# Optimization experiments

Hardware: AMD Instinct MI355X
Metric: run time of the kernel (lower is better)

## Reference

```python
import jax, jax.numpy as jnp
import numpy as np

N = 4096
Q_DIM = K_DIM = V_DIM = OUT_DIM = ATTN_DIM = 512
NUM_HEADS = 8
HEAD_DIM = ATTN_DIM // NUM_HEADS
SCALE = float(HEAD_DIM) ** (-0.5)


def setup_inputs() -> dict:
    key = jax.random.key(0)
    ks = jax.random.split(key, 12)
    def lin(kw, kb, out_d, in_d):
        bound = 1.0 / np.sqrt(in_d)
        w = jax.random.uniform(kw, (out_d, in_d), jnp.float32, -bound, bound)
        b = jax.random.uniform(kb, (out_d,), jnp.float32, -bound, bound)
        return w, b
    wq_w, wq_b = lin(ks[0], ks[1], ATTN_DIM, Q_DIM)
    wk_w, wk_b = lin(ks[2], ks[3], ATTN_DIM, K_DIM)
    wv_w, wv_b = lin(ks[4], ks[5], ATTN_DIM, V_DIM)
    wo_w, wo_b = lin(ks[6], ks[7], OUT_DIM, ATTN_DIM)
    q = jax.random.normal(ks[8], (N, Q_DIM), jnp.float32)
    k = jax.random.normal(ks[9], (N, K_DIM), jnp.float32)
    v = jax.random.normal(ks[10], (N, V_DIM), jnp.float32)
    mask = jax.random.uniform(ks[11], (N, N)) < 0.1  # True = masked out
    return {"q": q, "k": k, "v": v, "mask": mask,
            "wq_w": wq_w, "wq_b": wq_b, "wk_w": wk_w, "wk_b": wk_b,
            "wv_w": wv_w, "wv_b": wv_b, "wo_w": wo_w, "wo_b": wo_b}


def reference(q, k, v, mask, wq_w, wq_b, wk_w, wk_b, wv_w, wv_b, wo_w, wo_b):
    # Linear projections (torch Linear: x @ W.T + b)
    qp = q @ wq_w.T + wq_b  # (N, A)
    kp = k @ wk_w.T + wk_b
    vp = v @ wv_w.T + wv_b
    # (N, A) -> (H, N, dh)
    qh = qp.reshape(N, NUM_HEADS, HEAD_DIM).transpose(1, 0, 2)
    kh = kp.reshape(N, NUM_HEADS, HEAD_DIM).transpose(1, 0, 2)
    vh = vp.reshape(N, NUM_HEADS, HEAD_DIM).transpose(1, 0, 2)
    attn = jnp.einsum('hnd,hmd->hnm', qh, kh) * SCALE  # (H, N, N)
    attn = jnp.where(mask[None, :, :], jnp.float32(-1e6), attn)
    attn = jax.nn.softmax(attn, axis=-1)
    o = jnp.einsum('hnm,hmd->hnd', attn, vh)  # (H, N, dh)
    o = o.transpose(1, 0, 2).reshape(N, ATTN_DIM)
    return o @ wo_w.T + wo_b  # (N, out_dim)
```

## Files before the change

kernel.cpp:

```cpp
#include <hip/hip_runtime.h>


typedef __attribute__((ext_vector_type(8))) short bf16x8;
typedef __attribute__((ext_vector_type(4))) float f32x4;

#define N_TOK 4096
#define D_MODEL 512
#define QSCALE 0.18033688f

__device__ __forceinline__ unsigned short f2bf(float f) {
  unsigned u = __float_as_uint(f);
  return (unsigned short)((u + 0x7FFFu + ((u >> 16) & 1u)) >> 16);
}
__device__ __forceinline__ unsigned pack_bf16(float a, float b) {
  unsigned ua = __float_as_uint(a), ub = __float_as_uint(b);
  ua += 0x7FFFu + ((ua >> 16) & 1u);
  ub += 0x7FFFu + ((ub >> 16) & 1u);
  return (ua >> 16) | (ub & 0xFFFF0000u);
}
__device__ __forceinline__ f32x4 mfma16(bf16x8 a, bf16x8 b, f32x4 c) {
  return __builtin_amdgcn_mfma_f32_16x16x32_bf16(a, b, c, 0, 0, 0);
}
__device__ __forceinline__ float fast_exp2(float x) {
#if __has_builtin(__builtin_amdgcn_exp2f)
  return __builtin_amdgcn_exp2f(x);
#else
  return exp2f(x);
#endif
}

__global__ __launch_bounds__(256) void detect_kernel(
    const unsigned* __restrict__ mask, unsigned* __restrict__ flags) {
  __shared__ int s_bad;
  int t = threadIdx.x;
  if (t == 0) s_bad = 0;
  __syncthreads();
  int bad = 0;
  for (int i = t; i < 4096; i += 256)
    if (mask[i] > 1u) bad = 1;
  if (bad) atomicOr(&s_bad, 1);
  __syncthreads();
  if (t == 0) {
    flags[0] = 0;
    flags[1] = s_bad ? 1u : 0u;
  }
}

__global__ __launch_bounds__(256) void pack_mask_kernel(
    const void* __restrict__ m, unsigned long long* __restrict__ bits,
    const unsigned* __restrict__ flags) {
  int gt = blockIdx.x * 256 + threadIdx.x;
  int wave = gt >> 6;
  int lane = threadIdx.x & 63;
  int base = wave * 256;
  unsigned long long b0, b1, b2, b3;
  if (flags[1]) {
    const unsigned char* m8 = (const unsigned char*)m;
    b0 = __ballot(m8[base + 0 * 64 + lane] != 0);
    b1 = __ballot(m8[base + 1 * 64 + lane] != 0);
    b2 = __ballot(m8[base + 2 * 64 + lane] != 0);
    b3 = __ballot(m8[base + 3 * 64 + lane] != 0);
  } else {
    const int* m4 = (const int*)m;
    b0 = __ballot(m4[base + 0 * 64 + lane] != 0);
    b1 = __ballot(m4[base + 1 * 64 + lane] != 0);
    b2 = __ballot(m4[base + 2 * 64 + lane] != 0);
    b3 = __ballot(m4[base + 3 * 64 + lane] != 0);
  }
  if (lane < 4) {
    unsigned long long bl = lane == 0 ? b0 : lane == 1 ? b1 : lane == 2 ? b2 : b3;
    bits[wave * 4 + lane] = bl;
  }
}

template <int F32>
__device__ __forceinline__ void load16(const void* base, int idx,
                                       unsigned short* dst) {
  if (F32) {
    const float* p = (const float*)base + idx;
    float4 f0 = *(const float4*)(p + 0);
    float4 f1 = *(const float4*)(p + 4);
    float4 f2 = *(const float4*)(p + 8);
    float4 f3 = *(const float4*)(p + 12);
    unsigned* d = (unsigned*)dst;
    d[0] = pack_bf16(f0.x, f0.y); d[1] = pack_bf16(f0.z, f0.w);
    d[2] = pack_bf16(f1.x, f1.y); d[3] = pack_bf16(f1.z, f1.w);
    d[4] = pack_bf16(f2.x, f2.y); d[5] = pack_bf16(f2.z, f2.w);
    d[6] = pack_bf16(f3.x, f3.y); d[7] = pack_bf16(f3.z, f3.w);
  } else {
    const unsigned short* p = (const unsigned short*)base + idx;
    *(uint4*)dst = *(const uint4*)p;
    *(uint4*)(dst + 8) = *(const uint4*)(p + 8);
  }
}

template <int A32, int O32>
__device__ __forceinline__ void gemm_body(
    const void* __restrict__ A, const float* __restrict__ W,
    const float* __restrict__ bias, void* __restrict__ out, float oscale) {
  __shared__ unsigned short As[128 * 72];
  __shared__ unsigned short Bs[128 * 72];
  const int t = threadIdx.x;
  const int lane = t & 63, w = t >> 6;
  const int wm = w & 1, wn = w >> 1;
  const int q4 = lane >> 4, i15 = lane & 15;
  const int m0 = blockIdx.y * 128, n0 = blockIdx.x * 128;
  f32x4 acc[4][4] = {};
  const int sr = t >> 2;
  const int sc = (t & 3) * 16;
  for (int k0 = 0; k0 < 512; k0 += 64) {
    __syncthreads();
#pragma unroll
    for (int p = 0; p < 2; ++p) {
      int row = sr + p * 64;
      unsigned short ta[16], tb[16];
      load16<A32>(A, (m0 + row) * 512 + k0 + sc, ta);
      load16<1>(W, (n0 + row) * 512 + k0 + sc, tb);
      *(uint4*)(As + row * 72 + sc) = *(uint4*)ta;
      *(uint4*)(As + row * 72 + sc + 8) = *(uint4*)(ta + 8);
      *(uint4*)(Bs + row * 72 + sc) = *(uint4*)tb;
      *(uint4*)(Bs + row * 72 + sc + 8) = *(uint4*)(tb + 8);
    }
    __syncthreads();
#pragma unroll
    for (int ks = 0; ks < 2; ++ks) {
      bf16x8 af[4], bfr[4];
#pragma unroll
      for (int mt = 0; mt < 4; ++mt)
        af[mt] = *(const bf16x8*)(As + (wm * 64 + mt * 16 + i15) * 72 + q4 * 8 + ks * 32);
#pragma unroll
      for (int nt = 0; nt < 4; ++nt)
        bfr[nt] = *(const bf16x8*)(Bs + (wn * 64 + nt * 16 + i15) * 72 + q4 * 8 + ks * 32);
#pragma unroll
      for (int mt = 0; mt < 4; ++mt)
#pragma unroll
        for (int nt = 0; nt < 4; ++nt)
          acc[mt][nt] = mfma16(af[mt], bfr[nt], acc[mt][nt]);
    }
  }
#pragma unroll
  for (int nt = 0; nt < 4; ++nt) {
    int col = n0 + wn * 64 + nt * 16 + i15;
    float bv = bias[col];
#pragma unroll
    for (int mt = 0; mt < 4; ++mt) {
      int rowb = m0 + wm * 64 + mt * 16 + q4 * 4;
#pragma unroll
      for (int rr = 0; rr < 4; ++rr) {
        int idx = (rowb + rr) * 512 + col;
        float val = (acc[mt][nt][rr] + bv) * oscale;
        if (O32) ((float*)out)[idx] = val;
        else ((unsigned short*)out)[idx] = f2bf(val);
      }
    }
  }
}

__global__ __launch_bounds__(256) void qkv_gemm_kernel(
    const float* __restrict__ q, const float* __restrict__ k,
    const float* __restrict__ v, const float* __restrict__ wq,
    const float* __restrict__ wk, const float* __restrict__ wv,
    const float* __restrict__ bq, const float* __restrict__ bk,
    const float* __restrict__ bv, unsigned short* __restrict__ outbase) {
  int z = blockIdx.z;
  const float* A = z == 0 ? q : z == 1 ? k : v;
  const float* W = z == 0 ? wq : z == 1 ? wk : wv;
  const float* B = z == 0 ? bq : z == 1 ? bk : bv;
  float sc = z == 0 ? QSCALE : 1.0f;
  gemm_body<1, 0>(A, W, B, outbase + (size_t)z * (N_TOK * D_MODEL), sc);
}

__global__ __launch_bounds__(256) void out_gemm_kernel(
    const unsigned short* __restrict__ A, const float* __restrict__ W,
    const float* __restrict__ B, float* __restrict__ out) {
  gemm_body<0, 1>(A, W, B, out, 1.0f);
}

__global__ __launch_bounds__(256, 3) void attn_kernel(
    const unsigned short* __restrict__ qp, const unsigned short* __restrict__ kp,
    const unsigned short* __restrict__ vp,
    const unsigned long long* __restrict__ mbits,
    float* __restrict__ Op, float* __restrict__ dp) {
  __shared__ unsigned short Ks[128 * 64];
  __shared__ unsigned short Vt[64 * 128];
  const int t = threadIdx.x;
  const int lane = t & 63, w = t >> 6;
  const int q4 = lane >> 4, i15 = lane & 15;
  const int head = blockIdx.y;
  const int ch = head * 64;
  const int i0 = blockIdx.x * 128;
  const int iw = w * 32;
  const int bz = blockIdx.z;
  const int t0 = bz * 11;
  const int ntile = (bz < 2) ? 11 : 10;
  const int L0 = i15 + ((q4 & 1) << 5);
  const int L1 = L0 + 16;
  const bool oddsel = q4 >= 2;
  bf16x8 qf[2][2];
#pragma unroll
  for (int nt = 0; nt < 2; ++nt) {
    int ig = i0 + iw + nt * 16 + i15;
#pragma unroll
    for (int ksd = 0; ksd < 2; ++ksd)
      qf[nt][ksd] = *(const bf16x8*)(qp + ig * 512 + ch + q4 * 8 + ksd * 32);
  }
  const unsigned long long* mrow[2];
  mrow[0] = mbits + (size_t)(i0 + iw + i15) * 64;
  mrow[1] = mbits + (size_t)(i0 + iw + 16 + i15) * 64;
  f32x4 oacc[4][2] = {};
  float den[2] = {0.f, 0.f};
  for (int jt = 0; jt < ntile; ++jt) {
    const int j0 = (t0 + jt) * 128;
    __syncthreads();
    {
      int j = t >> 1;
      const unsigned short* src = kp + (j0 + j) * 512 + ch;
      int cb = (t & 1) * 4;
#pragma unroll
      for (int kk = 0; kk < 4; ++kk) {
        int g = cb + kk;
        uint4 vv = *(const uint4*)(src + g * 8);
        *(uint4*)(Ks + j * 64 + ((g ^ (j & 7)) * 8)) = vv;
      }
    }
    {
      int jp = t & 63;
      int d0 = (t >> 6) * 16;
      int j = jp * 2;
      const unsigned short* s0 = vp + (j0 + j) * 512 + ch + d0;
      uint4 va = *(const uint4*)(s0);
      uint4 vb = *(const uint4*)(s0 + 8);
      uint4 vc = *(const uint4*)(s0 + 512);
      uint4 vd = *(const uint4*)(s0 + 520);
      const unsigned short* ea = (const unsigned short*)&va;
      const unsigned short* eb = (const unsigned short*)&vb;
      const unsigned short* ec = (const unsigned short*)&vc;
      const unsigned short* ed = (const unsigned short*)&vd;
#pragma unroll
      for (int x = 0; x < 16; ++x) {
        int d = d0 + x;
        unsigned short lo = (x < 8) ? ea[x] : eb[x - 8];
        unsigned short hi = (x < 8) ? ec[x] : ed[x - 8];
        int gs = (j >> 3) ^ (d & 15);
        *(unsigned int*)(Vt + d * 128 + gs * 8 + (j & 7)) =
            (unsigned)lo | ((unsigned)hi << 16);
      }
    }
    unsigned long long mw[2][2];
#pragma unroll
    for (int nt = 0; nt < 2; ++nt) {
      mw[nt][0] = mrow[nt][(j0 >> 6) + 0];
      mw[nt][1] = mrow[nt][(j0 >> 6) + 1];
    }
    __syncthreads();
#pragma unroll
    for (int pr = 0; pr < 4; ++pr) {
      f32x4 sv[2][2] = {};
#pragma unroll
      for (int half = 0; half < 2; ++half) {
        int mt = pr * 2 + half;
        int j = mt * 16 + i15;
#pragma unroll
        for (int ksd = 0; ksd < 2; ++ksd) {
          int g = q4 + ksd * 4;
          bf16x8 a = *(const bf16x8*)(Ks + j * 64 + ((g ^ (j & 7)) * 8));
          sv[half][0] = mfma16(a, qf[0][ksd], sv[half][0]);
          sv[half][1] = mfma16(a, qf[1][ksd], sv[half][1]);
        }
      }
      uint2 pk[2][2];
#pragma unroll
      for (int half = 0; half < 2; ++half) {
        int mt = pr * 2 + half;
#pragma unroll
        for (int nt = 0; nt < 2; ++nt) {
          unsigned bits4 =
              (unsigned)(mw[nt][mt >> 2] >> ((mt & 3) * 16 + q4 * 4)) & 15u;
          float p0 = fast_exp2((bits4 & 1u) ? -200.f : sv[half][nt][0]);
          float p1 = fast_exp2((bits4 & 2u) ? -200.f : sv[half][nt][1]);
          float p2 = fast_exp2((bits4 & 4u) ? -200.f : sv[half][nt][2]);
          float p3 = fast_exp2((bits4 & 8u) ? -200.f : sv[half][nt][3]);
          den[nt] += (p0 + p1) + (p2 + p3);
          pk[half][nt].x = pack_bf16(p0, p1);
          pk[half][nt].y = pack_bf16(p2, p3);
        }
      }
      bf16x8 pf[2];
#pragma unroll
      for (int nt = 0; nt < 2; ++nt) {
        unsigned e0 = __shfl(pk[0][nt].x, L0), e1 = __shfl(pk[0][nt].y, L0);
        unsigned e2 = __shfl(pk[0][nt].x, L1), e3 = __shfl(pk[0][nt].y, L1);
        unsigned o0 = __shfl(pk[1][nt].x, L0), o1 = __shfl(pk[1][nt].y, L0);
        unsigned o2 = __shfl(pk[1][nt].x, L1), o3 = __shfl(pk[1][nt].y, L1);
        union { unsigned u[4]; bf16x8 v; } fb;
        fb.u[0] = oddsel ? o0 : e0;
        fb.u[1] = oddsel ? o1 : e1;
        fb.u[2] = oddsel ? o2 : e2;
        fb.u[3] = oddsel ? o3 : e3;
        pf[nt] = fb.v;
      }
#pragma unroll
      for (int mt = 0; mt < 4; ++mt) {
        int d = mt * 16 + i15;
        int g = pr * 4 + q4;
        bf16x8 vf = *(const bf16x8*)(Vt + d * 128 + ((g ^ (d & 15)) * 8));
        oacc[mt][0] = mfma16(vf, pf[0], oacc[mt][0]);
        oacc[mt][1] = mfma16(vf, pf[1], oacc[mt][1]);
      }
    }
  }
  float* Opc = Op + (size_t)bz * N_TOK * 512;
#pragma unroll
  for (int nt = 0; nt < 2; ++nt) {
    float d = den[nt];
    d += __shfl_xor(d, 16);
    d += __shfl_xor(d, 32);
    int ig = i0 + iw + nt * 16 + i15;
#pragma unroll
    for (int mt = 0; mt < 4; ++mt)
      *(f32x4*)(Opc + (size_t)ig * 512 + ch + mt * 16 + q4 * 4) = oacc[mt][nt];
    if (q4 == 0) dp[(bz * 8 + head) * N_TOK + ig] = d;
  }
}

__global__ __launch_bounds__(256) void reduce_kernel(
    const float* __restrict__ Op, const float* __restrict__ dp,
    unsigned short* __restrict__ ob) {
  int x = blockIdx.x * 256 + threadIdx.x;
  int i = x >> 7;
  int c = (x & 127) * 4;
  size_t off = (size_t)i * 512 + c;
  const size_t CH = (size_t)N_TOK * 512;
  float4 a0 = *(const float4*)(Op + off);
  float4 a1 = *(const float4*)(Op + CH + off);
  float4 a2 = *(const float4*)(Op + 2 * CH + off);
  int h = c >> 6;
  float den = dp[h * N_TOK + i] + dp[(8 + h) * N_TOK + i] + dp[(16 + h) * N_TOK + i];
  float inv = 1.0f / den;
  float sx = (a0.x + a1.x + a2.x) * inv;
  float sy = (a0.y + a1.y + a2.y) * inv;
  float sz = (a0.z + a1.z + a2.z) * inv;
  float sw = (a0.w + a1.w + a2.w) * inv;
  uint2 o;
  o.x = pack_bf16(sx, sy);
  o.y = pack_bf16(sz, sw);
  *(uint2*)(ob + off) = o;
}

extern "C" void kernel_launch(void* const* d_in, const int* in_sizes, int n_in,
                              void* d_out, int out_size, void* d_ws, size_t ws_size,
                              hipStream_t stream) {
  const float* q = (const float*)d_in[0];
  const float* k = (const float*)d_in[1];
  const float* v = (const float*)d_in[2];
  const void* mask = d_in[3];
  const float* wq = (const float*)d_in[4];
  const float* bq = (const float*)d_in[5];
  const float* wk = (const float*)d_in[6];
  const float* bk = (const float*)d_in[7];
  const float* wv = (const float*)d_in[8];
  const float* bv = (const float*)d_in[9];
  const float* wo = (const float*)d_in[10];
  const float* bo = (const float*)d_in[11];

  char* ws = (char*)d_ws;
  unsigned* flags = (unsigned*)ws;
  unsigned long long* mb = (unsigned long long*)(ws + 4096);
  unsigned short* qkvp = (unsigned short*)(ws + 4096 + (2ull << 20));
  unsigned short* ob = qkvp + 3ull * N_TOK * D_MODEL;
  float* Op = (float*)(ob + (size_t)N_TOK * D_MODEL);
  float* dp = Op + 3ull * N_TOK * 512;

  detect_kernel<<<1, 256, 0, stream>>>((const unsigned*)mask, flags);
  pack_mask_kernel<<<16384, 256, 0, stream>>>(mask, mb, flags);
  qkv_gemm_kernel<<<dim3(4, 32, 3), 256, 0, stream>>>(q, k, v, wq, wk, wv, bq,
                                                      bk, bv, qkvp);
  attn_kernel<<<dim3(32, 8, 3), 256, 0, stream>>>(
      qkvp, qkvp + (N_TOK * D_MODEL), qkvp + 2 * (N_TOK * D_MODEL), mb, Op, dp);
  reduce_kernel<<<2048, 256, 0, stream>>>(Op, dp, ob);
  out_gemm_kernel<<<dim3(4, 32), 256, 0, stream>>>(ob, wo, bo, (float*)d_out);
}
```

Before: 256.9 us.

## Restructure attention into single-wave blocks with register-prefetched K/V and transposed V

The attention kernel moves from 256-thread blocks over 128 query rows to single-wave blocks over 64 query rows, with the key range split into 4 chunks instead of 3. K and V tiles are prefetched into registers one tile ahead, and no block barriers are needed since each block is one wave. The V projection is now written transposed per head, so V tiles load without a per-element transpose, and the probability fragments feed the second MFMA directly without cross-lane shuffles. The trade-offs are an extra partial buffer and more reduce traffic, plus higher register pressure from prefetch and accumulators. The mask detection also now checks only 256 words instead of 4096.

```diff
diff --git a/kernel.cpp b/kernel.cpp
--- a/kernel.cpp
+++ b/kernel.cpp
@@ -5,7 +5,6 @@
 typedef __attribute__((ext_vector_type(4))) float f32x4;
 
 #define N_TOK 4096
-#define D_MODEL 512
 #define QSCALE 0.18033688f
 
 __device__ __forceinline__ unsigned short f2bf(float f) {
@@ -35,10 +34,7 @@
   int t = threadIdx.x;
   if (t == 0) s_bad = 0;
   __syncthreads();
-  int bad = 0;
-  for (int i = t; i < 4096; i += 256)
-    if (mask[i] > 1u) bad = 1;
-  if (bad) atomicOr(&s_bad, 1);
+  if (mask[t] > 1u) atomicOr(&s_bad, 1);
   __syncthreads();
   if (t == 0) {
     flags[0] = 0;
@@ -94,7 +90,7 @@
   }
 }
 
-template <int A32, int O32>
+template <int A32, int O32, int TRANS>
 __device__ __forceinline__ void gemm_body(
     const void* __restrict__ A, const float* __restrict__ W,
     const float* __restrict__ bias, void* __restrict__ out, float oscale) {
@@ -142,15 +138,29 @@
   for (int nt = 0; nt < 4; ++nt) {
     int col = n0 + wn * 64 + nt * 16 + i15;
     float bv = bias[col];
-#pragma unroll
-    for (int mt = 0; mt < 4; ++mt) {
-      int rowb = m0 + wm * 64 + mt * 16 + q4 * 4;
-#pragma unroll
-      for (int rr = 0; rr < 4; ++rr) {
-        int idx = (rowb + rr) * 512 + col;
-        float val = (acc[mt][nt][rr] + bv) * oscale;
-        if (O32) ((float*)out)[idx] = val;
-        else ((unsigned short*)out)[idx] = f2bf(val);
+    if (TRANS) {
+      unsigned short* ob_ = (unsigned short*)out +
+                            (size_t)(col >> 6) * (64 * N_TOK) +
+                            (size_t)(col & 63) * N_TOK;
+#pragma unroll
+      for (int mt = 0; mt < 4; ++mt) {
+        int rowb = m0 + wm * 64 + mt * 16 + q4 * 4;
+        uint2 pr;
+        pr.x = pack_bf16(acc[mt][nt][0] + bv, acc[mt][nt][1] + bv);
+        pr.y = pack_bf16(acc[mt][nt][2] + bv, acc[mt][nt][3] + bv);
+        *(uint2*)(ob_ + rowb) = pr;
+      }
+    } else {
+#pragma unroll
+      for (int mt = 0; mt < 4; ++mt) {
+        int rowb = m0 + wm * 64 + mt * 16 + q4 * 4;
+#pragma unroll
+        for (int rr = 0; rr < 4; ++rr) {
+          int idx = (rowb + rr) * 512 + col;
+          float val = (acc[mt][nt][rr] + bv) * oscale;
+          if (O32) ((float*)out)[idx] = val;
+          else ((unsigned short*)out)[idx] = f2bf(val);
+        }
       }
     }
   }
@@ -163,163 +173,158 @@
     const float* __restrict__ bq, const float* __restrict__ bk,
     const float* __restrict__ bv, unsigned short* __restrict__ outbase) {
   int z = blockIdx.z;
-  const float* A = z == 0 ? q : z == 1 ? k : v;
-  const float* W = z == 0 ? wq : z == 1 ? wk : wv;
-  const float* B = z == 0 ? bq : z == 1 ? bk : bv;
-  float sc = z == 0 ? QSCALE : 1.0f;
-  gemm_body<1, 0>(A, W, B, outbase + (size_t)z * (N_TOK * D_MODEL), sc);
+  if (z == 0) {
+    gemm_body<1, 0, 0>(q, wq, bq, outbase, QSCALE);
+  } else if (z == 1) {
+    gemm_body<1, 0, 0>(k, wk, bk, outbase + (size_t)N_TOK * 512, 1.0f);
+  } else {
+    gemm_body<1, 0, 1>(v, wv, bv, outbase + 2ull * N_TOK * 512, 1.0f);
+  }
 }
 
 __global__ __launch_bounds__(256) void out_gemm_kernel(
     const unsigned short* __restrict__ A, const float* __restrict__ W,
     const float* __restrict__ B, float* __restrict__ out) {
-  gemm_body<0, 1>(A, W, B, out, 1.0f);
-}
-
-__global__ __launch_bounds__(256, 3) void attn_kernel(
+  gemm_body<0, 1, 0>(A, W, B, out, 1.0f);
+}
+
+__global__ __launch_bounds__(64, 2) void attn_kernel(
     const unsigned short* __restrict__ qp, const unsigned short* __restrict__ kp,
-    const unsigned short* __restrict__ vp,
+    const unsigned short* __restrict__ vpT,
     const unsigned long long* __restrict__ mbits,
     float* __restrict__ Op, float* __restrict__ dp) {
-  __shared__ unsigned short Ks[128 * 64];
-  __shared__ unsigned short Vt[64 * 128];
-  const int t = threadIdx.x;
-  const int lane = t & 63, w = t >> 6;
-  const int q4 = lane >> 4, i15 = lane & 15;
-  const int head = blockIdx.y;
+  __shared__ unsigned short Ks[64 * 64];
+  __shared__ unsigned short Vt[64 * 64];
+  const int l = threadIdx.x;
+  const int q4 = l >> 4, i15 = l & 15;
+  const int bx = blockIdx.x;
+  const int ig = bx & 63;
+  const int head = (bx >> 6) & 7;
+  const int chunk = bx >> 9;
+  const int i0 = ig * 64;
   const int ch = head * 64;
-  const int i0 = blockIdx.x * 128;
-  const int iw = w * 32;
-  const int bz = blockIdx.z;
-  const int t0 = bz * 11;
-  const int ntile = (bz < 2) ? 11 : 10;
-  const int L0 = i15 + ((q4 & 1) << 5);
-  const int L1 = L0 + 16;
-  const bool oddsel = q4 >= 2;
-  bf16x8 qf[2][2];
-#pragma unroll
-  for (int nt = 0; nt < 2; ++nt) {
-    int ig = i0 + iw + nt * 16 + i15;
-#pragma unroll
-    for (int ksd = 0; ksd < 2; ++ksd)
-      qf[nt][ksd] = *(const bf16x8*)(qp + ig * 512 + ch + q4 * 8 + ksd * 32);
-  }
-  const unsigned long long* mrow[2];
-  mrow[0] = mbits + (size_t)(i0 + iw + i15) * 64;
-  mrow[1] = mbits + (size_t)(i0 + iw + 16 + i15) * 64;
-  f32x4 oacc[4][2] = {};
-  float den[2] = {0.f, 0.f};
-  for (int jt = 0; jt < ntile; ++jt) {
-    const int j0 = (t0 + jt) * 128;
-    __syncthreads();
+  const int ji = l >> 3;
+  const int sg = l & 7;
+  bf16x8 qf[4][2];
+#pragma unroll
+  for (int nt = 0; nt < 4; ++nt) {
+    const unsigned short* qr = qp + (size_t)(i0 + nt * 16 + i15) * 512 + ch;
+#pragma unroll
+    for (int ks = 0; ks < 2; ++ks)
+      qf[nt][ks] = *(const bf16x8*)(qr + ks * 32 + q4 * 8);
+  }
+  const unsigned long long* mrow[4];
+#pragma unroll
+  for (int nt = 0; nt < 4; ++nt)
+    mrow[nt] = mbits + (size_t)(i0 + nt * 16 + i15) * 64;
+  f32x4 oacc[4][4] = {};
+  float den[4] = {0.f, 0.f, 0.f, 0.f};
+  const unsigned short* vbase = vpT + (size_t)head * (64 * N_TOK);
+  uint4 kst[8], vst[8];
+  {
+    int j0 = chunk * 1024;
+#pragma unroll
+    for (int r = 0; r < 8; ++r) {
+      int row = r * 8 + ji;
+      kst[r] = *(const uint4*)(kp + (size_t)(j0 + row) * 512 + ch + sg * 8);
+      vst[r] = *(const uint4*)(vbase + (size_t)row * N_TOK + j0 + sg * 8);
+    }
+  }
+  for (int jt = 0; jt < 16; ++jt) {
+    const int j0 = chunk * 1024 + jt * 64;
+#pragma unroll
+    for (int r = 0; r < 8; ++r) {
+      int row = r * 8 + ji;
+      *(uint4*)(Ks + row * 64 + ((sg ^ ji ^ r) * 8)) = kst[r];
+      const unsigned* vs = (const unsigned*)&vst[r];
+#pragma unroll
+      for (int rr = 0; rr < 2; ++rr) {
+        int kg = (sg >> 2) * 4 + (sg & 1) * 2 + rr;
+        int hh = (sg >> 1) & 1;
+        *(uint2*)(Vt + row * 64 + ((kg ^ ji ^ r) * 8) + hh * 4) =
+            make_uint2(vs[rr * 2], vs[rr * 2 + 1]);
+      }
+    }
     {
-      int j = t >> 1;
-      const unsigned short* src = kp + (j0 + j) * 512 + ch;
-      int cb = (t & 1) * 4;
-#pragma unroll
-      for (int kk = 0; kk < 4; ++kk) {
-        int g = cb + kk;
-        uint4 vv = *(const uint4*)(src + g * 8);
-        *(uint4*)(Ks + j * 64 + ((g ^ (j & 7)) * 8)) = vv;
-      }
-    }
-    {
-      int jp = t & 63;
-      int d0 = (t >> 6) * 16;
-      int j = jp * 2;
-      const unsigned short* s0 = vp + (j0 + j) * 512 + ch + d0;
-      uint4 va = *(const uint4*)(s0);
-      uint4 vb = *(const uint4*)(s0 + 8);
-      uint4 vc = *(const uint4*)(s0 + 512);
-      uint4 vd = *(const uint4*)(s0 + 520);
-      const unsigned short* ea = (const unsigned short*)&va;
-      const unsigned short* eb = (const unsigned short*)&vb;
-      const unsigned short* ec = (const unsigned short*)&vc;
-      const unsigned short* ed = (const unsigned short*)&vd;
-#pragma unroll
-      for (int x = 0; x < 16; ++x) {
-        int d = d0 + x;
-        unsigned short lo = (x < 8) ? ea[x] : eb[x - 8];
-        unsigned short hi = (x < 8) ? ec[x] : ed[x - 8];
-        int gs = (j >> 3) ^ (d & 15);
-        *(unsigned int*)(Vt + d * 128 + gs * 8 + (j & 7)) =
-            (unsigned)lo | ((unsigned)hi << 16);
-      }
-    }
-    unsigned long long mw[2][2];
-#pragma unroll
-    for (int nt = 0; nt < 2; ++nt) {
-      mw[nt][0] = mrow[nt][(j0 >> 6) + 0];
-      mw[nt][1] = mrow[nt][(j0 >> 6) + 1];
-    }
-    __syncthreads();
-#pragma unroll
-    for (int pr = 0; pr < 4; ++pr) {
-      f32x4 sv[2][2] = {};
-#pragma unroll
-      for (int half = 0; half < 2; ++half) {
-        int mt = pr * 2 + half;
-        int j = mt * 16 + i15;
-#pragma unroll
-        for (int ksd = 0; ksd < 2; ++ksd) {
-          int g = q4 + ksd * 4;
-          bf16x8 a = *(const bf16x8*)(Ks + j * 64 + ((g ^ (j & 7)) * 8));
-          sv[half][0] = mfma16(a, qf[0][ksd], sv[half][0]);
-          sv[half][1] = mfma16(a, qf[1][ksd], sv[half][1]);
-        }
-      }
-      uint2 pk[2][2];
-#pragma unroll
-      for (int half = 0; half < 2; ++half) {
-        int mt = pr * 2 + half;
-#pragma unroll
-        for (int nt = 0; nt < 2; ++nt) {
-          unsigned bits4 =
-              (unsigned)(mw[nt][mt >> 2] >> ((mt & 3) * 16 + q4 * 4)) & 15u;
-          float p0 = fast_exp2((bits4 & 1u) ? -200.f : sv[half][nt][0]);
-          float p1 = fast_exp2((bits4 & 2u) ? -200.f : sv[half][nt][1]);
-          float p2 = fast_exp2((bits4 & 4u) ? -200.f : sv[half][nt][2]);
-          float p3 = fast_exp2((bits4 & 8u) ? -200.f : sv[half][nt][3]);
-          den[nt] += (p0 + p1) + (p2 + p3);
-          pk[half][nt].x = pack_bf16(p0, p1);
-          pk[half][nt].y = pack_bf16(p2, p3);
-        }
-      }
-      bf16x8 pf[2];
-#pragma unroll
-      for (int nt = 0; nt < 2; ++nt) {
-        unsigned e0 = __shfl(pk[0][nt].x, L0), e1 = __shfl(pk[0][nt].y, L0);
-        unsigned e2 = __shfl(pk[0][nt].x, L1), e3 = __shfl(pk[0][nt].y, L1);
-        unsigned o0 = __shfl(pk[1][nt].x, L0), o1 = __shfl(pk[1][nt].y, L0);
-        unsigned o2 = __shfl(pk[1][nt].x, L1), o3 = __shfl(pk[1][nt].y, L1);
-        union { unsigned u[4]; bf16x8 v; } fb;
-        fb.u[0] = oddsel ? o0 : e0;
-        fb.u[1] = oddsel ? o1 : e1;
-        fb.u[2] = oddsel ? o2 : e2;
-        fb.u[3] = oddsel ? o3 : e3;
-        pf[nt] = fb.v;
-      }
-#pragma unroll
-      for (int mt = 0; mt < 4; ++mt) {
-        int d = mt * 16 + i15;
-        int g = pr * 4 + q4;
-        bf16x8 vf = *(const bf16x8*)(Vt + d * 128 + ((g ^ (d & 15)) * 8));
-        oacc[mt][0] = mfma16(vf, pf[0], oacc[mt][0]);
-        oacc[mt][1] = mfma16(vf, pf[1], oacc[mt][1]);
-      }
-    }
-  }
-  float* Opc = Op + (size_t)bz * N_TOK * 512;
-#pragma unroll
-  for (int nt = 0; nt < 2; ++nt) {
-    float d = den[nt];
-    d += __shfl_xor(d, 16);
-    d += __shfl_xor(d, 32);
-    int ig = i0 + iw + nt * 16 + i15;
-#pragma unroll
-    for (int mt = 0; mt < 4; ++mt)
-      *(f32x4*)(Opc + (size_t)ig * 512 + ch + mt * 16 + q4 * 4) = oacc[mt][nt];
-    if (q4 == 0) dp[(bz * 8 + head) * N_TOK + ig] = d;
+      int jn = chunk * 1024 + ((jt + 1) & 15) * 64;
+#pragma unroll
+      for (int r = 0; r < 8; ++r) {
+        int row = r * 8 + ji;
+        kst[r] = *(const uint4*)(kp + (size_t)(jn + row) * 512 + ch + sg * 8);
+        vst[r] = *(const uint4*)(vbase + (size_t)row * N_TOK + jn + sg * 8);
+      }
+    }
+    unsigned long long mw[4];
+    int widx = j0 >> 6;
+#pragma unroll
+    for (int nt = 0; nt < 4; ++nt) mw[nt] = mrow[nt][widx];
+    bf16x8 Kf[4][2];
+#pragma unroll
+    for (int mtj = 0; mtj < 4; ++mtj) {
+      int js = mtj * 16 + i15;
+#pragma unroll
+      for (int ksd = 0; ksd < 2; ++ksd) {
+        int g = ksd * 4 + q4;
+        Kf[mtj][ksd] =
+            *(const bf16x8*)(Ks + js * 64 + ((g ^ (js & 7) ^ (js >> 3)) * 8));
+      }
+    }
+    unsigned pk[4][8];
+#pragma unroll
+    for (int nt = 0; nt < 4; ++nt) {
+      float dsum = 0.f;
+#pragma unroll
+      for (int mtj = 0; mtj < 4; ++mtj) {
+        f32x4 s = {0.f, 0.f, 0.f, 0.f};
+        s = mfma16(Kf[mtj][0], qf[nt][0], s);
+        s = mfma16(Kf[mtj][1], qf[nt][1], s);
+        unsigned nib = (unsigned)(mw[nt] >> (mtj * 16 + q4 * 4)) & 15u;
+        float p0 = fast_exp2((nib & 1u) ? -200.f : s[0]);
+        float p1 = fast_exp2((nib & 2u) ? -200.f : s[1]);
+        float p2 = fast_exp2((nib & 4u) ? -200.f : s[2]);
+        float p3 = fast_exp2((nib & 8u) ? -200.f : s[3]);
+        dsum += (p0 + p1) + (p2 + p3);
+        pk[nt][mtj * 2] = pack_bf16(p0, p1);
+        pk[nt][mtj * 2 + 1] = pack_bf16(p2, p3);
+      }
+      den[nt] += dsum;
+    }
+    bf16x8 Vf[2][4];
+#pragma unroll
+    for (int ks = 0; ks < 2; ++ks)
+#pragma unroll
+      for (int mtd = 0; mtd < 4; ++mtd) {
+        int d = mtd * 16 + i15;
+        int kg = ks * 4 + q4;
+        Vf[ks][mtd] =
+            *(const bf16x8*)(Vt + d * 64 + ((kg ^ (d & 7) ^ (d >> 3)) * 8));
+      }
+#pragma unroll
+    for (int nt = 0; nt < 4; ++nt) {
+      union { unsigned u[4]; bf16x8 v; } pf0, pf1;
+      pf0.u[0] = pk[nt][0]; pf0.u[1] = pk[nt][1];
+      pf0.u[2] = pk[nt][2]; pf0.u[3] = pk[nt][3];
+      pf1.u[0] = pk[nt][4]; pf1.u[1] = pk[nt][5];
+      pf1.u[2] = pk[nt][6]; pf1.u[3] = pk[nt][7];
+#pragma unroll
+      for (int mtd = 0; mtd < 4; ++mtd) {
+        oacc[mtd][nt] = mfma16(Vf[0][mtd], pf0.v, oacc[mtd][nt]);
+        oacc[mtd][nt] = mfma16(Vf[1][mtd], pf1.v, oacc[mtd][nt]);
+      }
+    }
+  }
+  float* Opc = Op + (size_t)chunk * N_TOK * 512;
+#pragma unroll
+  for (int nt = 0; nt < 4; ++nt) {
+    float dn = den[nt];
+    dn += __shfl_xor(dn, 16);
+    dn += __shfl_xor(dn, 32);
+    int row = i0 + nt * 16 + i15;
+#pragma unroll
+    for (int mtd = 0; mtd < 4; ++mtd)
+      *(f32x4*)(Opc + (size_t)row * 512 + ch + mtd * 16 + q4 * 4) =
+          oacc[mtd][nt];
+    if (q4 == 0) dp[(size_t)(chunk * 8 + head) * N_TOK + row] = dn;
   }
 }
 
@@ -334,13 +339,15 @@
   float4 a0 = *(const float4*)(Op + off);
   float4 a1 = *(const float4*)(Op + CH + off);
   float4 a2 = *(const float4*)(Op + 2 * CH + off);
+  float4 a3 = *(const float4*)(Op + 3 * CH + off);
   int h = c >> 6;
-  float den = dp[h * N_TOK + i] + dp[(8 + h) * N_TOK + i] + dp[(16 + h) * N_TOK + i];
+  float den = dp[(size_t)h * N_TOK + i] + dp[(size_t)(8 + h) * N_TOK + i] +
+              dp[(size_t)(16 + h) * N_TOK + i] + dp[(size_t)(24 + h) * N_TOK + i];
   float inv = 1.0f / den;
-  float sx = (a0.x + a1.x + a2.x) * inv;
-  float sy = (a0.y + a1.y + a2.y) * inv;
-  float sz = (a0.z + a1.z + a2.z) * inv;
-  float sw = (a0.w + a1.w + a2.w) * inv;
+  float sx = (a0.x + a1.x + a2.x + a3.x) * inv;
+  float sy = (a0.y + a1.y + a2.y + a3.y) * inv;
+  float sz = (a0.z + a1.z + a2.z + a3.z) * inv;
+  float sw = (a0.w + a1.w + a2.w + a3.w) * inv;
   uint2 o;
   o.x = pack_bf16(sx, sy);
   o.y = pack_bf16(sz, sw);
@@ -367,16 +374,16 @@
   unsigned* flags = (unsigned*)ws;
   unsigned long long* mb = (unsigned long long*)(ws + 4096);
   unsigned short* qkvp = (unsigned short*)(ws + 4096 + (2ull << 20));
-  unsigned short* ob = qkvp + 3ull * N_TOK * D_MODEL;
-  float* Op = (float*)(ob + (size_t)N_TOK * D_MODEL);
-  float* dp = Op + 3ull * N_TOK * 512;
+  unsigned short* ob = qkvp + 3ull * N_TOK * 512;
+  float* Op = (float*)(ob + (size_t)N_TOK * 512);
+  float* dp = Op + 4ull * N_TOK * 512;
 
   detect_kernel<<<1, 256, 0, stream>>>((const unsigned*)mask, flags);
   pack_mask_kernel<<<16384, 256, 0, stream>>>(mask, mb, flags);
   qkv_gemm_kernel<<<dim3(4, 32, 3), 256, 0, stream>>>(q, k, v, wq, wk, wv, bq,
                                                       bk, bv, qkvp);
-  attn_kernel<<<dim3(32, 8, 3), 256, 0, stream>>>(
-      qkvp, qkvp + (N_TOK * D_MODEL), qkvp + 2 * (N_TOK * D_MODEL), mb, Op, dp);
+  attn_kernel<<<2048, 64, 0, stream>>>(
+      qkvp, qkvp + (size_t)N_TOK * 512, qkvp + 2ull * N_TOK * 512, mb, Op, dp);
   reduce_kernel<<<2048, 256, 0, stream>>>(Op, dp, ob);
   out_gemm_kernel<<<dim3(4, 32), 256, 0, stream>>>(ob, wo, bo, (float*)d_out);
 }
```

Result: slower. 414.4 us (+61.3%).
